# Performance work log

Measured on AMD Instinct MI355X. Metric: run time of the kernel, lower is better.

The kernel has to match this reference:

```python
import jax, jax.numpy as jnp
import numpy as np

D_MODEL = 1024
N_HEADS = 16
D_K = 64

def setup_inputs() -> dict:
    key = jax.random.key(0)
    k0, k1, k2, k3, k4 = jax.random.split(key, 5)
    B, S = 4, 4096
    std = 0.02
    x = jax.random.normal(k0, (B, S, D_MODEL), dtype=jnp.float32)
    # nn.Linear weights are [out, in]; init normal(0, 0.02) as in _init_weights
    W_q = std * jax.random.normal(k1, (N_HEADS * D_K, D_MODEL), dtype=jnp.float32)
    W_k = std * jax.random.normal(k2, (N_HEADS * D_K, D_MODEL), dtype=jnp.float32)
    W_v = std * jax.random.normal(k3, (N_HEADS * D_K, D_MODEL), dtype=jnp.float32)
    W_o = std * jax.random.normal(k4, (D_MODEL, N_HEADS * D_K), dtype=jnp.float32)
    return {"x": x, "W_q": W_q, "W_k": W_k, "W_v": W_v, "W_o": W_o}

def reference(x, W_q, W_k, W_v, W_o):
    B, S, _ = x.shape
    H, Dk = N_HEADS, D_K
    # projections (nn.Linear: x @ W.T), reshape to [B, S, H, Dk]
    q = (x @ W_q.T).reshape(B, S, H, Dk)
    k = (x @ W_k.T).reshape(B, S, H, Dk)
    v = (x @ W_v.T).reshape(B, S, H, Dk)
    scale = 1.0 / jnp.sqrt(jnp.float32(Dk))
    # No softmax between the two matmuls -> reassociate (QK^T)V = Q(K^TV),
    # identical math, O(S*d^2) instead of O(S^2*d).
    kv = jnp.einsum('bshd,bshe->bhde', k, v)          # [B, H, Dk, Dk]
    attn = jnp.einsum('bshd,bhde->bshe', q, kv) * scale  # [B, S, H, Dk]
    out = attn.reshape(B, S, H * Dk) @ W_o.T
    return out
```

## Files before the change

### kernel.cpp

```cpp
#include <hip/hip_runtime.h>
#include <hip/hip_bf16.h>
#include <cstdint>


typedef __bf16 bf16x8 __attribute__((ext_vector_type(8)));
typedef float f32x4 __attribute__((ext_vector_type(4)));
typedef unsigned short ushort_t;
typedef unsigned short ushort8_t __attribute__((ext_vector_type(8)));

__device__ inline void gld_lds16(const void* g, void* l) {
    __builtin_amdgcn_global_load_lds(
        (const __attribute__((address_space(1))) unsigned int*)g,
        (__attribute__((address_space(3))) unsigned int*)l,
        16, 0, 0);
}

__device__ inline ushort_t f2bf(float f) {
    uint32_t u = __float_as_uint(f);
    uint32_t r = (u + 0x7fffu + ((u >> 16) & 1u)) >> 16;
    return (ushort_t)r;
}
__device__ inline float bf2f(ushort_t u) {
    return __uint_as_float((uint32_t)u << 16);
}

__global__ __launch_bounds__(256)
void prep(const float* __restrict__ x, const float* __restrict__ Wk,
          const float* __restrict__ Wv, const float* __restrict__ Wq,
          ushort_t* __restrict__ xb, ushort_t* __restrict__ xbT,
          ushort_t* __restrict__ wkv, ushort_t* __restrict__ wqT)
{
    __shared__ ushort_t lt[32 * 522];
    const int id = blockIdx.x;
    const int t  = threadIdx.x;

    if (id < 1024) {
        const int s0 = id * 16;
        float4 f[16];
#pragma unroll
        for (int c = 0; c < 8; ++c) {
            const int slot = c * 256 + t;
            const int row  = slot >> 7;
            const int col8 = (slot & 127) * 8;
            f[2 * c]     = *(const float4*)&x[(size_t)(s0 + row) * 1024 + col8];
            f[2 * c + 1] = *(const float4*)&x[(size_t)(s0 + row) * 1024 + col8 + 4];
        }
#pragma unroll
        for (int c = 0; c < 8; ++c) {
            const int slot = c * 256 + t;
            const int row  = slot >> 7;
            const int col8 = (slot & 127) * 8;
            ushort8_t o;
            o[0] = f2bf(f[2 * c].x);     o[1] = f2bf(f[2 * c].y);
            o[2] = f2bf(f[2 * c].z);     o[3] = f2bf(f[2 * c].w);
            o[4] = f2bf(f[2 * c + 1].x); o[5] = f2bf(f[2 * c + 1].y);
            o[6] = f2bf(f[2 * c + 1].z); o[7] = f2bf(f[2 * c + 1].w);
            *(ushort8_t*)&xb[(size_t)(s0 + row) * 1024 + col8] = o;
        }
        return;
    }

    if (id < 2048) {
        const int id2 = id - 1024;
        const int s0 = (id2 & 31) * 512;
        const int i0 = (id2 >> 5) * 32;

        float4 f[16];
#pragma unroll
        for (int c = 0; c < 16; ++c) {
            const int slot = c * 256 + t;
            const int sl = slot >> 3;
            const int d4 = (slot & 7) * 4;
            f[c] = *(const float4*)&x[(size_t)(s0 + sl) * 1024 + i0 + d4];
        }
#pragma unroll
        for (int c = 0; c < 16; ++c) {
            const int slot = c * 256 + t;
            const int sl = slot >> 3;
            const int d4 = (slot & 7) * 4;
            lt[(d4 + 0) * 522 + sl] = f2bf(f[c].x);
            lt[(d4 + 1) * 522 + sl] = f2bf(f[c].y);
            lt[(d4 + 2) * 522 + sl] = f2bf(f[c].z);
            lt[(d4 + 3) * 522 + sl] = f2bf(f[c].w);
        }
        __syncthreads();
#pragma unroll
        for (int c = 0; c < 8; ++c) {
            const int slot = c * 256 + t;
            const int d  = slot >> 6;
            const int s8 = (slot & 63) * 8;
            const ushort8_t v = *(const ushort8_t*)&lt[d * 522 + s8];
            *(ushort8_t*)&xbT[(size_t)(i0 + d) * 16384 + s0 + s8] = v;
        }
        return;
    }

    if (id < 2304) {
        const int q  = id - 2048;
        const int qq = (q < 128) ? q : q - 128;
        const float* src = (q < 128) ? Wk : Wv;
        float4 f[8];
#pragma unroll
        for (int c = 0; c < 8; ++c)
            f[c] = *(const float4*)&src[(size_t)qq * 8192 + c * 1024 + t * 4];
        ushort_t* d = wkv + (size_t)q * 8192;
#pragma unroll
        for (int c = 0; c < 8; ++c) {
            ushort4 o;
            o.x = f2bf(f[c].x); o.y = f2bf(f[c].y);
            o.z = f2bf(f[c].z); o.w = f2bf(f[c].w);
            *(ushort4*)&d[c * 1024 + t * 4] = o;
        }
        return;
    }

    const int id2 = id - 2304;
    const int r0 = (id2 >> 4) * 64;
    const int c0 = (id2 & 15) * 64;
    float4 f[4];
#pragma unroll
    for (int c = 0; c < 4; ++c) {
        const int idx = c * 256 + t;
        const int r = idx >> 4, c4 = (idx & 15) * 4;
        f[c] = *(const float4*)&Wq[(size_t)(r0 + r) * 1024 + c0 + c4];
    }
#pragma unroll
    for (int c = 0; c < 4; ++c) {
        const int idx = c * 256 + t;
        const int r = idx >> 4, c4 = (idx & 15) * 4;
        ushort4 o;
        o.x = f2bf(f[c].x); o.y = f2bf(f[c].y);
        o.z = f2bf(f[c].z); o.w = f2bf(f[c].w);
        *(uint32_t*)&lt[r * 66 + c4]     = (uint32_t)o.x | ((uint32_t)o.y << 16);
        *(uint32_t*)&lt[r * 66 + c4 + 2] = (uint32_t)o.z | ((uint32_t)o.w << 16);
    }
    __syncthreads();
#pragma unroll
    for (int c = 0; c < 4; ++c) {
        const int idx = c * 256 + t;
        const int ri = idx >> 4, s4 = (idx & 15) * 4;
        ushort4 o;
        o.x = lt[(s4 + 0) * 66 + ri];
        o.y = lt[(s4 + 1) * 66 + ri];
        o.z = lt[(s4 + 2) * 66 + ri];
        o.w = lt[(s4 + 3) * 66 + ri];
        *(ushort4*)&wqT[(size_t)(c0 + ri) * 1024 + r0 + s4] = o;
    }
}

template <typename OutT>
__global__ __launch_bounds__(256, 4)
void gemm_bt_n64(const ushort_t* __restrict__ A, int lda, long strideA,
                 const ushort_t* __restrict__ B, int ldb, long strideB,
                 OutT* __restrict__ C0, int ldc0, long strideC0, int K)
{
    __shared__ ushort_t lA[128 * 32];
    __shared__ ushort_t lB[64 * 32];

    const int t    = threadIdx.x;
    const int lane = t & 63;
    const int wid  = t >> 6;
    const int z    = blockIdx.z;

    A += (size_t)z * strideA;
    B += (size_t)z * strideB;

    const int m0 = blockIdx.x * 128;
    const int n0 = blockIdx.y * 64;

    const int wm = (wid >> 1) * 64;
    const int wn = (wid & 1) * 32;
    const int mr = lane & 15;
    const int q4 = lane >> 4;

    const int row_a = t >> 2;
    const int seg   = ((t & 3) ^ ((t >> 3) & 3)) * 8;
    const int csw   = (q4 ^ ((mr >> 1) & 3)) * 16;

    f32x4 acc[4][2] = {};

    for (int k0 = 0; k0 < K; k0 += 32) {
        __syncthreads();
        gld_lds16(A + (size_t)(m0 + row_a) * lda + k0 + seg,      (char*)lA + wid * 1024);
        gld_lds16(A + (size_t)(m0 + 64 + row_a) * lda + k0 + seg, (char*)lA + 4096 + wid * 1024);
        gld_lds16(B + (size_t)(n0 + row_a) * ldb + k0 + seg,      (char*)lB + wid * 1024);
        __syncthreads();

        bf16x8 af[4], bf[2];
#pragma unroll
        for (int i = 0; i < 4; ++i)
            af[i] = *(const bf16x8*)((const char*)lA + (wm + i * 16 + mr) * 64 + csw);
#pragma unroll
        for (int j = 0; j < 2; ++j)
            bf[j] = *(const bf16x8*)((const char*)lB + (wn + j * 16 + mr) * 64 + csw);
#pragma unroll
        for (int i = 0; i < 4; ++i)
#pragma unroll
            for (int j = 0; j < 2; ++j)
                acc[i][j] = __builtin_amdgcn_mfma_f32_16x16x32_bf16(af[i], bf[j], acc[i][j], 0, 0, 0);
    }

    OutT* Cw = C0 + (size_t)z * strideC0;
#pragma unroll
    for (int i = 0; i < 4; ++i) {
        const int rbase = m0 + wm + i * 16 + q4 * 4;
#pragma unroll
        for (int j = 0; j < 2; ++j) {
            const int col = n0 + wn + j * 16 + mr;
#pragma unroll
            for (int r = 0; r < 4; ++r) {
                const float v = acc[i][j][r];
                const size_t off = (size_t)(rbase + r) * ldc0 + col;
                if constexpr (sizeof(OutT) == 2) Cw[off] = f2bf(v);
                else                             Cw[off] = v;
            }
        }
    }
}

__global__ __launch_bounds__(256, 2)
void gemm_fin(const ushort_t* __restrict__ A, int lda, long strideA,
              const ushort_t* __restrict__ B, int ldb, long strideB,
              float* __restrict__ C, int ldc, long strideC, int K)
{
    __shared__ char lds[73728];

    const int t    = threadIdx.x;
    const int lane = t & 63;
    const int wid  = t >> 6;

    const int L  = blockIdx.x + (blockIdx.y << 4) + (blockIdx.z << 7);
    const int w  = ((L & 7) << 6) + (L >> 3);
    const int bx = w & 15, by = (w >> 4) & 7, z = w >> 7;

    A += (size_t)z * strideA;
    B += (size_t)z * strideB;

    const int m0 = bx * 256;
    const int n0 = by * 128;

    const int wr = wid >> 1;
    const int wn = wid & 1;
    const int mr = lane & 15;
    const int q4 = lane >> 4;

    const int NT = K >> 5;

    const int row_a = t >> 2;
    const int seg   = ((t & 3) ^ ((t >> 3) & 3)) * 8;
    const int csw   = (q4 ^ ((mr >> 1) & 3)) * 16;

    auto stage = [&](int tgt, int bsel) {
        if (tgt >= NT) return;
        char* base = lds + bsel * 24576 + wid * 1024;
        const ushort_t* gA = A + (size_t)(m0 + row_a) * lda + tgt * 32 + seg;
        gld_lds16(gA,                          base);
        gld_lds16(gA + ((size_t)lda << 6),     base + 4096);
        gld_lds16(gA + ((size_t)lda << 7),     base + 8192);
        gld_lds16(gA + (size_t)lda * 192,      base + 12288);
        const ushort_t* gB = B + (size_t)(n0 + row_a) * ldb + tgt * 32 + seg;
        gld_lds16(gB,                          base + 16384);
        gld_lds16(gB + ((size_t)ldb << 6),     base + 20480);
    };

    bf16x8 af[8], bf[4];
    f32x4 acc[8][4] = {};

    stage(0, 0);
    stage(1, 1);
    asm volatile("s_waitcnt vmcnt(6)" ::: "memory");
    __builtin_amdgcn_s_barrier();

    int cur = 0;
    for (int kt = 0; kt < NT; ++kt) {
        const char* buf = lds + cur * 24576;
#pragma unroll
        for (int i = 0; i < 8; ++i)
            af[i] = *(const bf16x8*)(buf + (wr * 128 + i * 16 + mr) * 64 + csw);
#pragma unroll
        for (int j = 0; j < 4; ++j)
            bf[j] = *(const bf16x8*)(buf + 16384 + (wn * 64 + j * 16 + mr) * 64 + csw);

        int b2 = cur + 2; if (b2 >= 3) b2 -= 3;
        stage(kt + 2, b2);

        asm volatile("s_waitcnt lgkmcnt(0)" ::: "memory");
        __builtin_amdgcn_sched_barrier(0);
        __builtin_amdgcn_s_setprio(1);
#pragma unroll
        for (int i = 0; i < 8; ++i)
#pragma unroll
            for (int j = 0; j < 4; ++j)
                acc[i][j] = __builtin_amdgcn_mfma_f32_16x16x32_bf16(
                    af[i], bf[j], acc[i][j], 0, 0, 0);
        __builtin_amdgcn_s_setprio(0);
        __builtin_amdgcn_sched_barrier(0);

        if (kt + 2 < NT)       asm volatile("s_waitcnt vmcnt(6)" ::: "memory");
        else if (kt + 2 == NT) asm volatile("s_waitcnt vmcnt(0)" ::: "memory");
        __builtin_amdgcn_s_barrier();
        if (++cur == 3) cur = 0;
    }

    float* Cw = C + (size_t)z * strideC;
#pragma unroll
    for (int i = 0; i < 8; ++i) {
        const int rbase = m0 + wr * 128 + i * 16 + q4 * 4;
#pragma unroll
        for (int j = 0; j < 4; ++j) {
            const int col = n0 + wn * 64 + j * 16 + mr;
#pragma unroll
            for (int r = 0; r < 4; ++r)
                Cw[(size_t)(rbase + r) * ldc + col] = acc[i][j][r];
        }
    }
}

__global__ __launch_bounds__(256, 2)
void gemm_gram3(const ushort_t* __restrict__ X, ushort_t* __restrict__ Gp)
{
    __shared__ char lds[49152];

    const int t    = threadIdx.x;
    const int lane = t & 63;
    const int wid  = t >> 6;

    const int z  = blockIdx.x;
    const int bb = z >> 2, ks = z & 3;

    int ti = 0, rem = blockIdx.y;
    while (rem >= 8 - ti) { rem -= 8 - ti; ++ti; }
    const int tj = ti + rem;
    const int m0 = ti * 128;
    const int n0 = tj * 128;

    const ushort_t* A = X + (size_t)bb * 4096 + (size_t)ks * 1024;
    const int NT = 32;

    const int wm = (wid >> 1) * 64;
    const int wn = (wid & 1) * 64;
    const int mr = lane & 15;
    const int q4 = lane >> 4;

    const int row_a = t >> 2;
    const int seg   = ((t & 3) ^ ((t >> 3) & 3)) * 8;
    const int csw   = (q4 ^ ((mr >> 1) & 3)) * 16;

    auto stage = [&](int tgt, int bsel) {
        if (tgt >= NT) return;
        char* base = lds + bsel * 16384 + wid * 1024;
        const ushort_t* gA = A + (size_t)(m0 + row_a) * 16384 + tgt * 32 + seg;
        gld_lds16(gA,                        base);
        gld_lds16(gA + ((size_t)16384 << 6), base + 4096);
        const ushort_t* gB = A + (size_t)(n0 + row_a) * 16384 + tgt * 32 + seg;
        gld_lds16(gB,                        base + 8192);
        gld_lds16(gB + ((size_t)16384 << 6), base + 12288);
    };

    bf16x8 af[4], bf[4];
    f32x4 acc[4][4] = {};

    stage(0, 0);
    stage(1, 1);
    asm volatile("s_waitcnt vmcnt(4)" ::: "memory");
    __builtin_amdgcn_s_barrier();

    int cur = 0;
    for (int kt = 0; kt < NT; ++kt) {
        const char* buf = lds + cur * 16384;
#pragma unroll
        for (int i = 0; i < 4; ++i)
            af[i] = *(const bf16x8*)(buf + (wm + i * 16 + mr) * 64 + csw);
#pragma unroll
        for (int j = 0; j < 4; ++j)
            bf[j] = *(const bf16x8*)(buf + 8192 + (wn + j * 16 + mr) * 64 + csw);

        int b2 = cur + 2; if (b2 >= 3) b2 -= 3;
        stage(kt + 2, b2);

        asm volatile("s_waitcnt lgkmcnt(0)" ::: "memory");
        __builtin_amdgcn_sched_barrier(0);
        __builtin_amdgcn_s_setprio(1);
#pragma unroll
        for (int i = 0; i < 4; ++i)
#pragma unroll
            for (int j = 0; j < 4; ++j)
                acc[i][j] = __builtin_amdgcn_mfma_f32_16x16x32_bf16(
                    af[i], bf[j], acc[i][j], 0, 0, 0);
        __builtin_amdgcn_s_setprio(0);
        __builtin_amdgcn_sched_barrier(0);

        if (kt + 2 < NT)       asm volatile("s_waitcnt vmcnt(4)" ::: "memory");
        else if (kt + 2 == NT) asm volatile("s_waitcnt vmcnt(0)" ::: "memory");
        __builtin_amdgcn_s_barrier();
        if (++cur == 3) cur = 0;
    }

    ushort_t* Cw = Gp + ((size_t)z << 20);
#pragma unroll
    for (int i = 0; i < 4; ++i) {
        const int rbase = m0 + wm + i * 16 + q4 * 4;
#pragma unroll
        for (int j = 0; j < 4; ++j) {
            const int col = n0 + wn + j * 16 + mr;
#pragma unroll
            for (int r = 0; r < 4; ++r)
                Cw[(size_t)(rbase + r) * 1024 + col] = f2bf(acc[i][j][r]);
        }
    }
}

__global__ __launch_bounds__(256)
void reduce_g_t(const ushort_t* __restrict__ Gp, ushort_t* __restrict__ G)
{
    __shared__ float acc[64 * 65];

    const int t  = threadIdx.x;
    const int b  = blockIdx.y;
    const int tr = blockIdx.x >> 4, tc = blockIdx.x & 15;
    const int sr = (tr <= tc) ? tr : tc;
    const int sc = (tr <= tc) ? tc : tr;
    const bool flip = tr > tc;

#pragma unroll
    for (int p = 0; p < 4; ++p) {
        const int idx = p * 256 + t;
        const int r = idx >> 4, c = (idx & 15) * 4;
        float a0 = 0.f, a1 = 0.f, a2 = 0.f, a3 = 0.f;
#pragma unroll
        for (int ksl = 0; ksl < 4; ++ksl) {
            const ushort4 u = *(const ushort4*)&Gp[((size_t)(b * 4 + ksl) << 20)
                                                   + (size_t)(sr * 64 + r) * 1024 + sc * 64 + c];
            a0 += bf2f(u.x); a1 += bf2f(u.y); a2 += bf2f(u.z); a3 += bf2f(u.w);
        }
        acc[r * 65 + c + 0] = a0;
        acc[r * 65 + c + 1] = a1;
        acc[r * 65 + c + 2] = a2;
        acc[r * 65 + c + 3] = a3;
    }
    __syncthreads();

#pragma unroll
    for (int p = 0; p < 4; ++p) {
        const int idx = p * 256 + t;
        const int r = idx >> 4, c = (idx & 15) * 4;
        float v0, v1, v2, v3;
        if (flip) {
            v0 = acc[(c + 0) * 65 + r];
            v1 = acc[(c + 1) * 65 + r];
            v2 = acc[(c + 2) * 65 + r];
            v3 = acc[(c + 3) * 65 + r];
        } else {
            v0 = acc[r * 65 + c + 0];
            v1 = acc[r * 65 + c + 1];
            v2 = acc[r * 65 + c + 2];
            v3 = acc[r * 65 + c + 3];
        }
        ushort4 o;
        o.x = f2bf(v0); o.y = f2bf(v1); o.z = f2bf(v2); o.w = f2bf(v3);
        *(ushort4*)&G[((size_t)b << 20) + (size_t)(tr * 64 + r) * 1024 + tc * 64 + c] = o;
    }
}

__global__ __launch_bounds__(256)
void kvblk(const ushort_t* __restrict__ H, const ushort_t* __restrict__ Wv,
           float* __restrict__ KVp)
{
    __shared__ ushort_t sH[64 * 132];
    __shared__ ushort_t sV[64 * 132];

    const int t  = threadIdx.x;
    const int is = blockIdx.x;
    const int bh = blockIdx.y;
    const int b  = bh >> 4, h = bh & 15;

    const ushort_t* Hp = H + ((size_t)b << 20) + (size_t)(h * 64) * 1024 + is * 128;
    const ushort_t* Vp = Wv + (size_t)(h * 64) * 1024 + is * 128;

#pragma unroll
    for (int i2 = 0; i2 < 8; ++i2) {
        const int ci = i2 * 256 + t;
        const int r = ci >> 5, c = (ci & 31) * 4;
        *(uint2*)&sH[r * 132 + c] = *(const uint2*)&Hp[(size_t)r * 1024 + c];
        *(uint2*)&sV[r * 132 + c] = *(const uint2*)&Vp[(size_t)r * 1024 + c];
    }
    __syncthreads();

    const int d0 = (t >> 4) * 4;
    const int e0 = (t & 15) * 4;
    float acc[4][4] = {};

#pragma unroll 2
    for (int i4 = 0; i4 < 128; i4 += 4) {
        uint2 hu[4], vu[4];
#pragma unroll
        for (int j = 0; j < 4; ++j) {
            hu[j] = *(const uint2*)&sH[(d0 + j) * 132 + i4];
            vu[j] = *(const uint2*)&sV[(e0 + j) * 132 + i4];
        }
        float hf[4][4], vf[4][4];
#pragma unroll
        for (int j = 0; j < 4; ++j) {
            hf[j][0] = __uint_as_float(hu[j].x << 16);
            hf[j][1] = __uint_as_float(hu[j].x & 0xffff0000u);
            hf[j][2] = __uint_as_float(hu[j].y << 16);
            hf[j][3] = __uint_as_float(hu[j].y & 0xffff0000u);
            vf[j][0] = __uint_as_float(vu[j].x << 16);
            vf[j][1] = __uint_as_float(vu[j].x & 0xffff0000u);
            vf[j][2] = __uint_as_float(vu[j].y << 16);
            vf[j][3] = __uint_as_float(vu[j].y & 0xffff0000u);
        }
#pragma unroll
        for (int ii = 0; ii < 4; ++ii)
#pragma unroll
            for (int di = 0; di < 4; ++di)
#pragma unroll
                for (int ej = 0; ej < 4; ++ej)
                    acc[di][ej] += hf[di][ii] * vf[ej][ii];
    }

    float* outp = KVp + ((size_t)(is * 64 + bh)) * 4096;
#pragma unroll
    for (int i = 0; i < 4; ++i) {
        float4 o; o.x = acc[i][0]; o.y = acc[i][1]; o.z = acc[i][2]; o.w = acc[i][3];
        *(float4*)&outp[(d0 + i) * 64 + e0] = o;
    }
}

__global__ __launch_bounds__(256)
void make_E8(const float* __restrict__ KVp, const float* __restrict__ Wo,
             ushort_t* __restrict__ Et)
{
    __shared__ float skv[64 * 65];
    __shared__ float swo[64 * 65];

    const int t  = threadIdx.x;
    const int bh = blockIdx.y;
    const int b  = bh >> 4, h = bh & 15;
    const int j0 = blockIdx.x * 64;

#pragma unroll
    for (int i = 0; i < 4; ++i) {
        const int idx = t + i * 256;
        const int r = idx >> 4, c = (idx & 15) * 4;
        float4 f; f.x = 0.f; f.y = 0.f; f.z = 0.f; f.w = 0.f;
#pragma unroll
        for (int is = 0; is < 8; ++is) {
            const float4 p = *(const float4*)&KVp[((size_t)(is * 64 + bh)) * 4096
                                                  + r * 64 + c];
            f.x += p.x; f.y += p.y; f.z += p.z; f.w += p.w;
        }
        skv[r * 65 + c + 0] = f.x;
        skv[r * 65 + c + 1] = f.y;
        skv[r * 65 + c + 2] = f.z;
        skv[r * 65 + c + 3] = f.w;
        const float4 g = *(const float4*)&Wo[(size_t)(j0 + r) * 1024 + h * 64 + c];
        swo[r * 65 + c + 0] = g.x;
        swo[r * 65 + c + 1] = g.y;
        swo[r * 65 + c + 2] = g.z;
        swo[r * 65 + c + 3] = g.w;
    }
    __syncthreads();

    const int d0 = (t & 15) * 4;
#pragma unroll
    for (int pass = 0; pass < 4; ++pass) {
        const int jloc = (t >> 4) + pass * 16;
        float s0 = 0.f, s1 = 0.f, s2 = 0.f, s3 = 0.f;
        const float* wrow = &swo[jloc * 65];
#pragma unroll 8
        for (int e = 0; e < 64; ++e) {
            const float w = wrow[e];
            s0 += skv[(d0 + 0) * 65 + e] * w;
            s1 += skv[(d0 + 1) * 65 + e] * w;
            s2 += skv[(d0 + 2) * 65 + e] * w;
            s3 += skv[(d0 + 3) * 65 + e] * w;
        }
        ushort4 o;
        o.x = f2bf(s0 * 0.125f);
        o.y = f2bf(s1 * 0.125f);
        o.z = f2bf(s2 * 0.125f);
        o.w = f2bf(s3 * 0.125f);
        *(ushort4*)&Et[((size_t)b * 1024 + j0 + jloc) * 1024 + h * 64 + d0] = o;
    }
}


extern "C" void kernel_launch(void* const* d_in, const int* in_sizes, int n_in,
                              void* d_out, int out_size, void* d_ws, size_t ws_size,
                              hipStream_t stream)
{
    const float* x  = (const float*)d_in[0];
    const float* Wq = (const float*)d_in[1];
    const float* Wk = (const float*)d_in[2];
    const float* Wv = (const float*)d_in[3];
    const float* Wo = (const float*)d_in[4];
    float* out = (float*)d_out;

    const int B = 4, S = 4096, D = 1024;
    const long MB1 = 1048576;

    char* ws = (char*)d_ws;
    size_t off = 0;
    auto alloc = [&](size_t bytes) -> void* {
        void* p = ws + off;
        off += (bytes + 255) & ~(size_t)255;
        return p;
    };
    ushort_t* xb   = (ushort_t*)alloc((size_t)B * S * D * 2);
    ushort_t* xbT  = (ushort_t*)alloc((size_t)D * B * S * 2);
    ushort_t* wkv  = (ushort_t*)alloc((size_t)2 * D * D * 2);
    ushort_t* wqT  = (ushort_t*)alloc((size_t)D * D * 2);
    ushort_t* Gb   = (ushort_t*)alloc((size_t)B * D * D * 2);
    float*    kvp  = (float*)alloc((size_t)8 * 64 * 4096 * 4);
    ushort_t* Fb   = (ushort_t*)alloc((size_t)B * D * D * 2);
    char*     R1   = (char*)alloc((size_t)16 * MB1 * 2);
    ushort_t* Gp = (ushort_t*)R1;
    ushort_t* Hb = (ushort_t*)R1;
    ushort_t* Et = (ushort_t*)(R1 + 8 * MB1 * 2);
    ushort_t* wkb = wkv;
    ushort_t* wvb = wkv + MB1;

    prep<<<dim3(2560), dim3(256), 0, stream>>>(x, Wk, Wv, Wq, xb, xbT, wkv, wqT);

    gemm_gram3<<<dim3(16, 36), dim3(256), 0, stream>>>(xbT, Gp);
    reduce_g_t<<<dim3(256, 4), dim3(256), 0, stream>>>(Gp, Gb);

    gemm_bt_n64<ushort_t><<<dim3(8, 16, 4), dim3(256), 0, stream>>>(
        wkb, D, 0, Gb, D, MB1, Hb, D, MB1, D);

    kvblk<<<dim3(8, 64), dim3(256), 0, stream>>>(Hb, wvb, kvp);

    make_E8<<<dim3(16, 64), dim3(256), 0, stream>>>(kvp, Wo, Et);

    gemm_bt_n64<ushort_t><<<dim3(8, 16, 4), dim3(256), 0, stream>>>(
        Et, D, MB1, wqT, D, 0, Fb, D, (long)D * D, D);

    gemm_fin<<<dim3(16, 8, 4), dim3(256), 0, stream>>>(
        xb, D, (long)S * D, Fb, D, (long)D * D, out, D, (long)S * D, D);
}
```

Before: 309.7 us.

## Fuse bf16 conversion and transpose of x into one pass over input

The prep kernel now reads each 256x256 tile of x once. It writes the row-major bf16 copy directly and stages the same tile in a 128KB swizzled shared-memory buffer to emit the transposed copy. This removes the second full read of the fp32 input that the separate conversion and transpose blocks did. The trade-off is very large LDS use per block, which limits occupancy, and the transpose reads are scalar 16-bit LDS loads.

```diff
diff --git a/kernel.cpp b/kernel.cpp
--- a/kernel.cpp
+++ b/kernel.cpp
@@ -30,73 +30,59 @@
           ushort_t* __restrict__ xb, ushort_t* __restrict__ xbT,
           ushort_t* __restrict__ wkv, ushort_t* __restrict__ wqT)
 {
-    __shared__ ushort_t lt[32 * 522];
+    __shared__ ushort_t lt[256 * 256];
     const int id = blockIdx.x;
     const int t  = threadIdx.x;
 
-    if (id < 1024) {
-        const int s0 = id * 16;
-        float4 f[16];
-#pragma unroll
-        for (int c = 0; c < 8; ++c) {
-            const int slot = c * 256 + t;
-            const int row  = slot >> 7;
-            const int col8 = (slot & 127) * 8;
-            f[2 * c]     = *(const float4*)&x[(size_t)(s0 + row) * 1024 + col8];
-            f[2 * c + 1] = *(const float4*)&x[(size_t)(s0 + row) * 1024 + col8 + 4];
-        }
-#pragma unroll
-        for (int c = 0; c < 8; ++c) {
-            const int slot = c * 256 + t;
-            const int row  = slot >> 7;
-            const int col8 = (slot & 127) * 8;
-            ushort8_t o;
-            o[0] = f2bf(f[2 * c].x);     o[1] = f2bf(f[2 * c].y);
-            o[2] = f2bf(f[2 * c].z);     o[3] = f2bf(f[2 * c].w);
-            o[4] = f2bf(f[2 * c + 1].x); o[5] = f2bf(f[2 * c + 1].y);
-            o[6] = f2bf(f[2 * c + 1].z); o[7] = f2bf(f[2 * c + 1].w);
-            *(ushort8_t*)&xb[(size_t)(s0 + row) * 1024 + col8] = o;
-        }
-        return;
-    }
-
-    if (id < 2048) {
-        const int id2 = id - 1024;
-        const int s0 = (id2 & 31) * 512;
-        const int i0 = (id2 >> 5) * 32;
-
-        float4 f[16];
-#pragma unroll
+    if (id < 256) {
+        const int s0 = (id & 63) * 256;
+        const int i0 = (id >> 6) * 256;
+        auto lidx = [&](int s, int i) -> int {
+            return s * 256 + ((((i >> 3) ^ ((s >> 4) & 31)) << 3) | (i & 7));
+        };
+
         for (int c = 0; c < 16; ++c) {
             const int slot = c * 256 + t;
-            const int sl = slot >> 3;
-            const int d4 = (slot & 7) * 4;
-            f[c] = *(const float4*)&x[(size_t)(s0 + sl) * 1024 + i0 + d4];
-        }
-#pragma unroll
+            const int sr = slot >> 4;
+            const int fc = (slot & 15) * 16;
+            const float* xp = &x[(size_t)(s0 + sr) * 1024 + i0 + fc];
+            const float4 a = *(const float4*)(xp);
+            const float4 b = *(const float4*)(xp + 4);
+            const float4 d = *(const float4*)(xp + 8);
+            const float4 e = *(const float4*)(xp + 12);
+            ushort8_t o0, o1;
+            o0[0] = f2bf(a.x); o0[1] = f2bf(a.y); o0[2] = f2bf(a.z); o0[3] = f2bf(a.w);
+            o0[4] = f2bf(b.x); o0[5] = f2bf(b.y); o0[6] = f2bf(b.z); o0[7] = f2bf(b.w);
+            o1[0] = f2bf(d.x); o1[1] = f2bf(d.y); o1[2] = f2bf(d.z); o1[3] = f2bf(d.w);
+            o1[4] = f2bf(e.x); o1[5] = f2bf(e.y); o1[6] = f2bf(e.z); o1[7] = f2bf(e.w);
+            ushort_t* xo = &xb[(size_t)(s0 + sr) * 1024 + i0 + fc];
+            *(ushort8_t*)(xo)     = o0;
+            *(ushort8_t*)(xo + 8) = o1;
+            *(ushort8_t*)&lt[lidx(sr, fc)]     = o0;
+            *(ushort8_t*)&lt[lidx(sr, fc + 8)] = o1;
+        }
+        __syncthreads();
+
         for (int c = 0; c < 16; ++c) {
             const int slot = c * 256 + t;
-            const int sl = slot >> 3;
-            const int d4 = (slot & 7) * 4;
-            lt[(d4 + 0) * 522 + sl] = f2bf(f[c].x);
-            lt[(d4 + 1) * 522 + sl] = f2bf(f[c].y);
-            lt[(d4 + 2) * 522 + sl] = f2bf(f[c].z);
-            lt[(d4 + 3) * 522 + sl] = f2bf(f[c].w);
-        }
-        __syncthreads();
-#pragma unroll
-        for (int c = 0; c < 8; ++c) {
-            const int slot = c * 256 + t;
-            const int d  = slot >> 6;
-            const int s8 = (slot & 63) * 8;
-            const ushort8_t v = *(const ushort8_t*)&lt[d * 522 + s8];
-            *(ushort8_t*)&xbT[(size_t)(i0 + d) * 16384 + s0 + s8] = v;
+            const int ir = slot >> 4;
+            const int sc = (slot & 15) * 16;
+            ushort8_t o0, o1;
+#pragma unroll
+            for (int k = 0; k < 8; ++k)
+                o0[k] = lt[lidx(sc + k, ir)];
+#pragma unroll
+            for (int k = 0; k < 8; ++k)
+                o1[k] = lt[lidx(sc + 8 + k, ir)];
+            ushort_t* to = &xbT[(size_t)(i0 + ir) * 16384 + s0 + sc];
+            *(ushort8_t*)(to)     = o0;
+            *(ushort8_t*)(to + 8) = o1;
         }
         return;
     }
 
-    if (id < 2304) {
-        const int q  = id - 2048;
+    if (id < 512) {
+        const int q  = id - 256;
         const int qq = (q < 128) ? q : q - 128;
         const float* src = (q < 128) ? Wk : Wv;
         float4 f[8];
@@ -114,7 +100,7 @@
         return;
     }
 
-    const int id2 = id - 2304;
+    const int id2 = id - 512;
     const int r0 = (id2 >> 4) * 64;
     const int c0 = (id2 & 15) * 64;
     float4 f[4];
@@ -621,7 +607,7 @@
     ushort_t* wkb = wkv;
     ushort_t* wvb = wkv + MB1;
 
-    prep<<<dim3(2560), dim3(256), 0, stream>>>(x, Wk, Wv, Wq, xb, xbT, wkv, wqT);
+    prep<<<dim3(768), dim3(256), 0, stream>>>(x, Wk, Wv, Wq, xb, xbT, wkv, wqT);
 
     gemm_gram3<<<dim3(16, 36), dim3(256), 0, stream>>>(xbT, Gp);
     reduce_g_t<<<dim3(256, 4), dim3(256), 0, stream>>>(Gp, Gb);
```

Result: no change. 307.6 us (-0.7%).
